# Kernel tuning notes

Measured on AMD Instinct MI355X. Metric: run time of the kernel, lower is better.

## Reference

```python
import jax, jax.numpy as jnp
import numpy as np

# Sizes
NC, NT, NP = 100000, 300000, 50000   # customers, transactions, products
F, DIMC = 8, 16                      # columns per table, per-column embed dim
D = F * DIMC                         # 128 = proj_dim (lazy SAGEConv in-channels)
L, R = 2, 4                          # gnn layers, relation types
OUT = 10                             # out_channels
EM, EI = 300000, 600000              # edges: customer-makes-transaction, product-in-transaction


def setup_inputs() -> dict:
    key = jax.random.key(0)
    ks = jax.random.split(key, 14)
    s = 0.05
    return {
        "x_c": jax.random.normal(ks[0], (NC, F), jnp.float32),
        "x_t": jax.random.normal(ks[1], (NT, F), jnp.float32),
        "x_p": jax.random.normal(ks[2], (NP, F), jnp.float32),
        # per-table per-column numeric embedders: scalar -> DIMC (w*x + b)
        "W_col": jax.random.normal(ks[3], (3, F, DIMC), jnp.float32) * s,
        "b_col": jax.random.normal(ks[4], (3, F, DIMC), jnp.float32) * s,
        # SAGEConv weights per layer per relation: lin_l (neighbor) and lin_r (root)
        "Wn": jax.random.normal(ks[5], (L, R, D, D), jnp.float32) * s,
        "Wr": jax.random.normal(ks[6], (L, R, D, D), jnp.float32) * s,
        "b_lin": jax.random.normal(ks[7], (L, R, D), jnp.float32) * s,
        "W_out": jax.random.normal(ks[8], (D, OUT), jnp.float32) * s,
        "b_out": jax.random.normal(ks[9], (OUT,), jnp.float32) * s,
        "e_makes_src": jax.random.randint(ks[10], (EM,), 0, NC, jnp.int32),
        "e_makes_dst": jax.random.randint(ks[11], (EM,), 0, NT, jnp.int32),
        "e_in_src": jax.random.randint(ks[12], (EI,), 0, NP, jnp.int32),
        "e_in_dst": jax.random.randint(ks[13], (EI,), 0, NT, jnp.int32),
    }


def _embed(x, W, b):
    # x: [N, F]; W,b: [F, DIMC] -> [N, F*DIMC] (concat of per-column embeddings)
    n = x.shape[0]
    return (x[:, :, None] * W[None] + b[None]).reshape(n, -1)


def _sage(x_src, x_dst, src, dst, Wn, Wr, b, n_dst):
    # SAGEConv(mean): out = mean_neigh(x_src) @ Wn + b + x_dst @ Wr
    msg = jax.ops.segment_sum(x_src[src], dst, num_segments=n_dst)
    cnt = jax.ops.segment_sum(jnp.ones(src.shape[0], x_src.dtype), dst, num_segments=n_dst)
    mean = msg / jnp.maximum(cnt, 1.0)[:, None]  # isolated nodes -> 0 message
    return mean @ Wn + x_dst @ Wr + b


def reference(x_c, x_t, x_p, W_col, b_col, Wn, Wr, b_lin, W_out, b_out,
              e_makes_src, e_makes_dst, e_in_src, e_in_dst):
    h_c = _embed(x_c, W_col[0], b_col[0])
    h_t = _embed(x_t, W_col[1], b_col[1])
    h_p = _embed(x_p, W_col[2], b_col[2])
    for l in range(L):
        # R0: customer -makes-> transaction
        o_t0 = _sage(h_c, h_t, e_makes_src, e_makes_dst, Wn[l, 0], Wr[l, 0], b_lin[l, 0], NT)
        # R1: transaction -rev_makes-> customer
        o_c = _sage(h_t, h_c, e_makes_dst, e_makes_src, Wn[l, 1], Wr[l, 1], b_lin[l, 1], NC)
        # R2: product -in-> transaction
        o_t2 = _sage(h_p, h_t, e_in_src, e_in_dst, Wn[l, 2], Wr[l, 2], b_lin[l, 2], NT)
        # R3: transaction -rev_in-> product
        o_p = _sage(h_t, h_p, e_in_dst, e_in_src, Wn[l, 3], Wr[l, 3], b_lin[l, 3], NP)
        # HeteroConv(aggr='mean'): mean over relations targeting each dst type
        h_c, h_t, h_p = o_c, 0.5 * (o_t0 + o_t2), o_p
    logits = h_t @ W_out + b_out  # target_table = 'transaction'
    return jax.nn.softmax(logits, axis=1)
```

## Files before the change

kernel.cpp:

```cpp
#include <hip/hip_runtime.h>

#define NCV 100000
#define NTV 300000
#define NPV 50000
#define DD 128
#define OUTC 10
#define EMV 300000
#define EIV 600000
#define YST 16

__global__ __launch_bounds__(256) void prep_T_w(
    const float* __restrict__ Wn10, const float* __restrict__ Wn12,
    const float* __restrict__ Wr10, const float* __restrict__ Wr12,
    const float* __restrict__ Wout, float* __restrict__ T) {
  int gw = (blockIdx.x * 256 + threadIdx.x) >> 6;
  int lane = threadIdx.x & 63;
  if (gw >= 3 * 1280) return;
  int mat = gw / 1280, r = gw % 1280, n = r / 10, o = r % 10;
  float s = 0.f;
  #pragma unroll
  for (int mi = 0; mi < 2; ++mi) {
    int m = lane + mi * 64;
    float w;
    if (mat == 0) w = Wn10[n * 128 + m];
    else if (mat == 1) w = Wn12[n * 128 + m];
    else w = 0.5f * (Wr10[n * 128 + m] + Wr12[n * 128 + m]);
    s += w * Wout[m * 10 + o];
  }
  #pragma unroll
  for (int d = 32; d; d >>= 1) s += __shfl_xor(s, d);
  if (lane == 0) T[gw] = s;
}

__global__ __launch_bounds__(256) void prep_Q_w(
    const float* __restrict__ Wn01, const float* __restrict__ Wr01,
    const float* __restrict__ Wn03, const float* __restrict__ Wr03,
    const float* __restrict__ Wn00, const float* __restrict__ Wn02,
    const float* __restrict__ Wr00, const float* __restrict__ Wr02,
    const float* __restrict__ T, float* __restrict__ Q) {
  int gw = (blockIdx.x * 256 + threadIdx.x) >> 6;
  int lane = threadIdx.x & 63;
  if (gw >= 7 * 1280) return;
  int q = gw / 1280, r = gw % 1280, k = r / 10, o = r % 10;
  const float* T1 = T, *T2 = T + 1280, *T3 = T + 2560;
  float s = 0.f;
  #pragma unroll
  for (int ni = 0; ni < 2; ++ni) {
    int n = lane + ni * 64;
    float w, t;
    switch (q) {
      case 0: w = Wn01[k * 128 + n]; t = T1[n * 10 + o]; break;
      case 1: w = Wr01[k * 128 + n]; t = T1[n * 10 + o]; break;
      case 2: w = Wn03[k * 128 + n]; t = T2[n * 10 + o]; break;
      case 3: w = Wr03[k * 128 + n]; t = T2[n * 10 + o]; break;
      case 4: w = Wn00[k * 128 + n]; t = T3[n * 10 + o]; break;
      case 5: w = Wn02[k * 128 + n]; t = T3[n * 10 + o]; break;
      default: w = Wr00[k * 128 + n] + Wr02[k * 128 + n]; t = T3[n * 10 + o]; break;
    }
    s += w * t;
  }
  #pragma unroll
  for (int d = 32; d; d >>= 1) s += __shfl_xor(s, d);
  if (lane == 0) Q[gw] = s;
}

__global__ __launch_bounds__(256) void prep_B_w(
    const float* __restrict__ Wcol, const float* __restrict__ bcol,
    const float* __restrict__ b_lin, const float* __restrict__ Wout,
    const float* __restrict__ bout, const float* __restrict__ T,
    const float* __restrict__ Q, float* __restrict__ B) {
  int gw = (blockIdx.x * 256 + threadIdx.x) >> 6;
  int lane = threadIdx.x & 63;
  if (gw >= 450) return;
  int r = gw / 10, o = gw % 10;
  const float* WcC = Wcol, *WcT = Wcol + 128, *WcP = Wcol + 256;
  const float* bC = bcol, *bT = bcol + 128, *bP = bcol + 256;
  const float* Q1 = Q, *Q2 = Q + 1280, *Q3 = Q + 2560, *Q4 = Q + 3840;
  const float* Q5 = Q + 5120, *Q6 = Q + 6400, *Q7 = Q + 7680;
  const float* T1 = T, *T2 = T + 1280, *T3 = T + 2560;
  const float* b00 = b_lin, *b01 = b_lin + 128, *b02 = b_lin + 256, *b03 = b_lin + 384;
  const float* b10 = b_lin + 512, *b12 = b_lin + 768;
  float s = 0.f;
  if (r < 8) {
    if (lane < 16) s = WcT[r * 16 + lane] * Q1[(r * 16 + lane) * 10 + o];
  } else if (r < 16) {
    int j = r - 8;
    if (lane < 16)
      s = WcC[j * 16 + lane] * (Q2[(j * 16 + lane) * 10 + o] + Q5[(j * 16 + lane) * 10 + o]);
  } else if (r == 16) {
    for (int k2 = lane; k2 < 128; k2 += 64) s += bT[k2] * Q1[k2 * 10 + o];
  } else if (r < 25) {
    int j = r - 17;
    if (lane < 16) s = WcT[j * 16 + lane] * Q3[(j * 16 + lane) * 10 + o];
  } else if (r < 33) {
    int j = r - 25;
    if (lane < 16)
      s = WcP[j * 16 + lane] * (Q4[(j * 16 + lane) * 10 + o] + Q6[(j * 16 + lane) * 10 + o]);
  } else if (r == 33) {
    for (int k2 = lane; k2 < 128; k2 += 64) s += bT[k2] * Q3[k2 * 10 + o];
  } else if (r < 42) {
    int j = r - 34;
    if (lane < 16) s = WcT[j * 16 + lane] * Q7[(j * 16 + lane) * 10 + o];
  } else if (r == 42) {
    for (int k2 = lane; k2 < 128; k2 += 64)
      s += bC[k2] * (Q2[k2 * 10 + o] + Q5[k2 * 10 + o]) + b01[k2] * T1[k2 * 10 + o];
  } else if (r == 43) {
    for (int k2 = lane; k2 < 128; k2 += 64)
      s += bP[k2] * (Q4[k2 * 10 + o] + Q6[k2 * 10 + o]) + b03[k2] * T2[k2 * 10 + o];
  } else {
    for (int n = lane; n < 128; n += 64)
      s += (b10[n] + b12[n]) * Wout[n * 10 + o] + bT[n] * Q7[n * 10 + o] +
           (b00[n] + b02[n]) * T3[n * 10 + o];
  }
  #pragma unroll
  for (int d = 32; d; d >>= 1) s += __shfl_xor(s, d);
  if (lane == 0) {
    float v = s * 0.5f;
    if (r == 44) v += bout[o];
    B[gw] = v;
  }
}

__global__ __launch_bounds__(256) void build_lists(
    const int* __restrict__ ems, const int* __restrict__ emd,
    const int* __restrict__ eis, const int* __restrict__ eid,
    int* __restrict__ head_c, int* __restrict__ head_tm,
    int* __restrict__ head_p, int* __restrict__ head_ti,
    int* __restrict__ nxt_mc, int* __restrict__ nxt_mt,
    int* __restrict__ nxt_ip, int* __restrict__ nxt_it) {
  int e = blockIdx.x * 256 + threadIdx.x;
  if (e < EMV) {
    int c = ems[e], t = emd[e];
    nxt_mc[e] = atomicExch(&head_c[c], e);
    nxt_mt[e] = atomicExch(&head_tm[t], e);
  }
  if (e < EIV) {
    int p = eis[e], t = eid[e];
    nxt_ip[e] = atomicExch(&head_p[p], e);
    nxt_it[e] = atomicExch(&head_ti[t], e);
  }
}

__global__ __launch_bounds__(256) void gather_y(
    const float* __restrict__ xt,
    const int* __restrict__ emd, const int* __restrict__ eid,
    const int* __restrict__ head_c, const int* __restrict__ head_p,
    const int* __restrict__ nxt_mc, const int* __restrict__ nxt_ip,
    const float* __restrict__ xc, const float* __restrict__ xp,
    const float* __restrict__ B,
    float* __restrict__ y_c, float* __restrict__ y_p) {
  __shared__ float sB[340];
  int tid = threadIdx.x;
  for (int i = tid; i < 340; i += 256) sB[i] = B[i];
  __syncthreads();
  int i = blockIdx.x * 256 + tid;
  if (i >= NCV + NPV) return;
  bool isC = i < NCV;
  int idx = isC ? i : i - NCV;
  const int* dstA = isC ? emd : eid;
  const int* nxt = isC ? nxt_mc : nxt_ip;
  int e = isC ? head_c[idx] : head_p[idx];

  float acc[8] = {0.f, 0.f, 0.f, 0.f, 0.f, 0.f, 0.f, 0.f};
  float cnt = 0.f;
  while (e >= 0) {
    const float4* xr = (const float4*)(xt + (size_t)dstA[e] * 8);
    float4 u = xr[0], v = xr[1];
    acc[0] += u.x; acc[1] += u.y; acc[2] += u.z; acc[3] += u.w;
    acc[4] += v.x; acc[5] += v.y; acc[6] += v.z; acc[7] += v.w;
    cnt += 1.f;
    e = nxt[e];
  }

  const float* xo = (isC ? xc : xp) + (size_t)idx * 8;
  const float* Bs = sB + (isC ? 0 : 170);
  float g = cnt > 0.f ? 1.f : 0.f;
  float inv = g / fmaxf(cnt, 1.f);
  float lg[OUTC];
  #pragma unroll
  for (int o = 0; o < OUTC; ++o) lg[o] = g * Bs[16 * 10 + o];
  #pragma unroll
  for (int r = 0; r < 8; ++r) {
    float zb = acc[r] * inv;
    float zo = xo[r];
    #pragma unroll
    for (int o = 0; o < OUTC; ++o)
      lg[o] += zb * Bs[r * 10 + o] + zo * Bs[(8 + r) * 10 + o];
  }
  float* y = (isC ? y_c : y_p) + (size_t)idx * YST;
  #pragma unroll
  for (int o = 0; o < OUTC; ++o) y[o] = lg[o];
}

__global__ __launch_bounds__(256) void gather_t(
    const float* __restrict__ y_c, const float* __restrict__ y_p,
    const float* __restrict__ xt,
    const int* __restrict__ ems, const int* __restrict__ eis,
    const int* __restrict__ head_tm, const int* __restrict__ head_ti,
    const int* __restrict__ nxt_mt, const int* __restrict__ nxt_it,
    const float* __restrict__ B, float* __restrict__ out) {
  __shared__ float sB[110];
  int tid = threadIdx.x;
  for (int i = tid; i < 110; i += 256) sB[i] = B[340 + i];
  __syncthreads();
  int t = blockIdx.x * 256 + tid;
  if (t >= NTV) return;

  float sc[OUTC] = {0.f, 0.f, 0.f, 0.f, 0.f, 0.f, 0.f, 0.f, 0.f, 0.f};
  float sp[OUTC] = {0.f, 0.f, 0.f, 0.f, 0.f, 0.f, 0.f, 0.f, 0.f, 0.f};
  float dc = 0.f, dp = 0.f;
  for (int e = head_tm[t]; e >= 0; e = nxt_mt[e]) {
    const float* yr = y_c + (size_t)ems[e] * YST;
    float4 u = *(const float4*)yr;
    float4 v = *(const float4*)(yr + 4);
    float2 w = *(const float2*)(yr + 8);
    sc[0] += u.x; sc[1] += u.y; sc[2] += u.z; sc[3] += u.w;
    sc[4] += v.x; sc[5] += v.y; sc[6] += v.z; sc[7] += v.w;
    sc[8] += w.x; sc[9] += w.y;
    dc += 1.f;
  }
  for (int e = head_ti[t]; e >= 0; e = nxt_it[e]) {
    const float* yr = y_p + (size_t)eis[e] * YST;
    float4 u = *(const float4*)yr;
    float4 v = *(const float4*)(yr + 4);
    float2 w = *(const float2*)(yr + 8);
    sp[0] += u.x; sp[1] += u.y; sp[2] += u.z; sp[3] += u.w;
    sp[4] += v.x; sp[5] += v.y; sp[6] += v.z; sp[7] += v.w;
    sp[8] += w.x; sp[9] += w.y;
    dp += 1.f;
  }

  float Gc = dc > 0.f ? 1.f : 0.f, Gp = dp > 0.f ? 1.f : 0.f;
  float ivc = 1.f / fmaxf(dc, 1.f), ivp = 1.f / fmaxf(dp, 1.f);

  const float4* xp4 = (const float4*)(xt + (size_t)t * 8);
  float4 xa = xp4[0], xb = xp4[1];
  float xv[8] = {xa.x, xa.y, xa.z, xa.w, xb.x, xb.y, xb.z, xb.w};

  float lg[OUTC];
  #pragma unroll
  for (int o = 0; o < OUTC; ++o)
    lg[o] = sc[o] * ivc + sp[o] * ivp +
            Gc * sB[80 + o] + Gp * sB[90 + o] + sB[100 + o];
  #pragma unroll
  for (int r = 0; r < 8; ++r) {
    float xr = xv[r];
    #pragma unroll
    for (int o = 0; o < OUTC; ++o) lg[o] += xr * sB[r * 10 + o];
  }

  float m = lg[0];
  #pragma unroll
  for (int o = 1; o < OUTC; ++o) m = fmaxf(m, lg[o]);
  float s = 0.f;
  #pragma unroll
  for (int o = 0; o < OUTC; ++o) { lg[o] = __expf(lg[o] - m); s += lg[o]; }
  float invs = 1.0f / s;
  float* op = &out[(size_t)t * OUTC];
  #pragma unroll
  for (int o = 0; o < 5; ++o) {
    float2 p2; p2.x = lg[2 * o] * invs; p2.y = lg[2 * o + 1] * invs;
    *(float2*)&op[2 * o] = p2;
  }
}

extern "C" void kernel_launch(void* const* d_in, const int* in_sizes, int n_in,
                              void* d_out, int out_size, void* d_ws, size_t ws_size,
                              hipStream_t stream) {
  const float* x_c   = (const float*)d_in[0];
  const float* x_t   = (const float*)d_in[1];
  const float* x_p   = (const float*)d_in[2];
  const float* W_col = (const float*)d_in[3];
  const float* b_col = (const float*)d_in[4];
  const float* Wn    = (const float*)d_in[5];
  const float* Wr    = (const float*)d_in[6];
  const float* b_lin = (const float*)d_in[7];
  const float* W_out = (const float*)d_in[8];
  const float* b_out = (const float*)d_in[9];
  const int* e_m_src = (const int*)d_in[10];
  const int* e_m_dst = (const int*)d_in[11];
  const int* e_i_src = (const int*)d_in[12];
  const int* e_i_dst = (const int*)d_in[13];
  float* out = (float*)d_out;

  size_t cursor = 0;
  char* base = (char*)d_ws;
  auto alloc = [&](size_t bytes) {
    void* p = base + cursor;
    cursor += (bytes + 255) & ~(size_t)255;
    return p;
  };
  float* y_c  = (float*)alloc((size_t)NCV * YST * 4);
  float* y_p  = (float*)alloc((size_t)NPV * YST * 4);
  int* heads  = (int*)alloc((size_t)(NCV + NPV + 2 * NTV) * 4);
  int* head_c  = heads;
  int* head_p  = heads + NCV;
  int* head_tm = heads + NCV + NPV;
  int* head_ti = heads + NCV + NPV + NTV;
  int* nxt_mc = (int*)alloc((size_t)EMV * 4);
  int* nxt_mt = (int*)alloc((size_t)EMV * 4);
  int* nxt_ip = (int*)alloc((size_t)EIV * 4);
  int* nxt_it = (int*)alloc((size_t)EIV * 4);
  float* T    = (float*)alloc(3 * 1280 * 4);
  float* Q    = (float*)alloc(7 * 1280 * 4);
  float* B    = (float*)alloc(450 * 4);

  const float* Wn_l[2][4]; const float* Wr_l[2][4];
  for (int l = 0; l < 2; ++l)
    for (int r = 0; r < 4; ++r) {
      Wn_l[l][r] = Wn + (size_t)(l * 4 + r) * DD * DD;
      Wr_l[l][r] = Wr + (size_t)(l * 4 + r) * DD * DD;
    }

  hipMemsetAsync(heads, 0xFF, (size_t)(NCV + NPV + 2 * NTV) * 4, stream);

  prep_T_w<<<(3 * 1280 * 64 + 255) / 256, 256, 0, stream>>>(
      Wn_l[1][0], Wn_l[1][2], Wr_l[1][0], Wr_l[1][2], W_out, T);
  prep_Q_w<<<(7 * 1280 * 64 + 255) / 256, 256, 0, stream>>>(
      Wn_l[0][1], Wr_l[0][1], Wn_l[0][3], Wr_l[0][3],
      Wn_l[0][0], Wn_l[0][2], Wr_l[0][0], Wr_l[0][2], T, Q);
  prep_B_w<<<(450 * 64 + 255) / 256, 256, 0, stream>>>(
      W_col, b_col, b_lin, W_out, b_out, T, Q, B);

  build_lists<<<(EIV + 255) / 256, 256, 0, stream>>>(
      e_m_src, e_m_dst, e_i_src, e_i_dst,
      head_c, head_tm, head_p, head_ti,
      nxt_mc, nxt_mt, nxt_ip, nxt_it);

  gather_y<<<(NCV + NPV + 255) / 256, 256, 0, stream>>>(
      x_t, e_m_dst, e_i_dst, head_c, head_p, nxt_mc, nxt_ip,
      x_c, x_p, B, y_c, y_p);

  gather_t<<<(NTV + 255) / 256, 256, 0, stream>>>(
      y_c, y_p, x_t, e_m_src, e_i_src, head_tm, head_ti,
      nxt_mt, nxt_it, B, out);
}
```

Baseline: 245.0 us.

## Fuse weight folding and head init into one kernel; vectorize list building

```diff
diff --git a/kernel.cpp b/kernel.cpp
--- a/kernel.cpp
+++ b/kernel.cpp
@@ -3,121 +3,139 @@
 #define NCV 100000
 #define NTV 300000
 #define NPV 50000
-#define DD 128
 #define OUTC 10
 #define EMV 300000
 #define EIV 600000
 #define YST 16
 
-__global__ __launch_bounds__(256) void prep_T_w(
-    const float* __restrict__ Wn10, const float* __restrict__ Wn12,
-    const float* __restrict__ Wr10, const float* __restrict__ Wr12,
-    const float* __restrict__ Wout, float* __restrict__ T) {
-  int gw = (blockIdx.x * 256 + threadIdx.x) >> 6;
-  int lane = threadIdx.x & 63;
-  if (gw >= 3 * 1280) return;
-  int mat = gw / 1280, r = gw % 1280, n = r / 10, o = r % 10;
-  float s = 0.f;
-  #pragma unroll
-  for (int mi = 0; mi < 2; ++mi) {
-    int m = lane + mi * 64;
-    float w;
-    if (mat == 0) w = Wn10[n * 128 + m];
-    else if (mat == 1) w = Wn12[n * 128 + m];
-    else w = 0.5f * (Wr10[n * 128 + m] + Wr12[n * 128 + m]);
-    s += w * Wout[m * 10 + o];
-  }
-  #pragma unroll
-  for (int d = 32; d; d >>= 1) s += __shfl_xor(s, d);
-  if (lane == 0) T[gw] = s;
-}
-
-__global__ __launch_bounds__(256) void prep_Q_w(
-    const float* __restrict__ Wn01, const float* __restrict__ Wr01,
-    const float* __restrict__ Wn03, const float* __restrict__ Wr03,
-    const float* __restrict__ Wn00, const float* __restrict__ Wn02,
-    const float* __restrict__ Wr00, const float* __restrict__ Wr02,
-    const float* __restrict__ T, float* __restrict__ Q) {
-  int gw = (blockIdx.x * 256 + threadIdx.x) >> 6;
-  int lane = threadIdx.x & 63;
-  if (gw >= 7 * 1280) return;
-  int q = gw / 1280, r = gw % 1280, k = r / 10, o = r % 10;
-  const float* T1 = T, *T2 = T + 1280, *T3 = T + 2560;
-  float s = 0.f;
-  #pragma unroll
-  for (int ni = 0; ni < 2; ++ni) {
-    int n = lane + ni * 64;
-    float w, t;
-    switch (q) {
-      case 0: w = Wn01[k * 128 + n]; t = T1[n * 10 + o]; break;
-      case 1: w = Wr01[k * 128 + n]; t = T1[n * 10 + o]; break;
-      case 2: w = Wn03[k * 128 + n]; t = T2[n * 10 + o]; break;
-      case 3: w = Wr03[k * 128 + n]; t = T2[n * 10 + o]; break;
-      case 4: w = Wn00[k * 128 + n]; t = T3[n * 10 + o]; break;
-      case 5: w = Wn02[k * 128 + n]; t = T3[n * 10 + o]; break;
-      default: w = Wr00[k * 128 + n] + Wr02[k * 128 + n]; t = T3[n * 10 + o]; break;
+__global__ __launch_bounds__(256) void fold_init(
+    const float* __restrict__ Wcol, const float* __restrict__ bcol,
+    const float* __restrict__ Wn, const float* __restrict__ Wr,
+    const float* __restrict__ b_lin, const float* __restrict__ Wout,
+    const float* __restrict__ bout,
+    int* __restrict__ heads, int nheads, float* __restrict__ B) {
+  __shared__ float sWout[1280];
+  __shared__ float sT[3840];
+  __shared__ float sQ[8960];
+  int tid = threadIdx.x;
+
+  if (blockIdx.x != 0) {
+    int i = (blockIdx.x - 1) * 256 + tid;
+    int stride = (gridDim.x - 1) * 256;
+    for (; i < nheads; i += stride) heads[i] = -1;
+    return;
+  }
+
+  for (int i = tid; i < 1280; i += 256) sWout[i] = Wout[i];
+  __syncthreads();
+
+  const float* Wn00 = Wn;             const float* Wn01 = Wn + 1 * 16384;
+  const float* Wn02 = Wn + 2 * 16384; const float* Wn03 = Wn + 3 * 16384;
+  const float* Wn10 = Wn + 4 * 16384; const float* Wn12 = Wn + 6 * 16384;
+  const float* Wr00 = Wr;             const float* Wr01 = Wr + 1 * 16384;
+  const float* Wr02 = Wr + 2 * 16384; const float* Wr03 = Wr + 3 * 16384;
+  const float* Wr10 = Wr + 4 * 16384; const float* Wr12 = Wr + 6 * 16384;
+
+  for (int task = tid; task < 3 * 128; task += 256) {
+    int mat = task >> 7, n = task & 127;
+    float acc[10];
+    #pragma unroll
+    for (int o = 0; o < 10; ++o) acc[o] = 0.f;
+    for (int m = 0; m < 128; m += 4) {
+      float4 w4;
+      if (mat == 0) w4 = *(const float4*)(Wn10 + n * 128 + m);
+      else if (mat == 1) w4 = *(const float4*)(Wn12 + n * 128 + m);
+      else {
+        float4 a = *(const float4*)(Wr10 + n * 128 + m);
+        float4 b = *(const float4*)(Wr12 + n * 128 + m);
+        w4 = make_float4(0.5f * (a.x + b.x), 0.5f * (a.y + b.y),
+                         0.5f * (a.z + b.z), 0.5f * (a.w + b.w));
+      }
+      const float* wo = &sWout[m * 10];
+      #pragma unroll
+      for (int o = 0; o < 10; ++o)
+        acc[o] += w4.x * wo[o] + w4.y * wo[10 + o] + w4.z * wo[20 + o] + w4.w * wo[30 + o];
     }
-    s += w * t;
-  }
-  #pragma unroll
-  for (int d = 32; d; d >>= 1) s += __shfl_xor(s, d);
-  if (lane == 0) Q[gw] = s;
-}
-
-__global__ __launch_bounds__(256) void prep_B_w(
-    const float* __restrict__ Wcol, const float* __restrict__ bcol,
-    const float* __restrict__ b_lin, const float* __restrict__ Wout,
-    const float* __restrict__ bout, const float* __restrict__ T,
-    const float* __restrict__ Q, float* __restrict__ B) {
-  int gw = (blockIdx.x * 256 + threadIdx.x) >> 6;
-  int lane = threadIdx.x & 63;
-  if (gw >= 450) return;
-  int r = gw / 10, o = gw % 10;
+    #pragma unroll
+    for (int o = 0; o < 10; ++o) sT[task * 10 + o] = acc[o];
+  }
+  __syncthreads();
+
+  for (int task = tid; task < 7 * 128; task += 256) {
+    int q = task / 128, k = task & 127;
+    const float* Tsel = &sT[(q < 2 ? 0 : (q < 4 ? 1 : 2)) * 1280];
+    float acc[10];
+    #pragma unroll
+    for (int o = 0; o < 10; ++o) acc[o] = 0.f;
+    for (int n = 0; n < 128; n += 4) {
+      float4 w4;
+      switch (q) {
+        case 0: w4 = *(const float4*)(Wn01 + k * 128 + n); break;
+        case 1: w4 = *(const float4*)(Wr01 + k * 128 + n); break;
+        case 2: w4 = *(const float4*)(Wn03 + k * 128 + n); break;
+        case 3: w4 = *(const float4*)(Wr03 + k * 128 + n); break;
+        case 4: w4 = *(const float4*)(Wn00 + k * 128 + n); break;
+        case 5: w4 = *(const float4*)(Wn02 + k * 128 + n); break;
+        default: {
+          float4 a = *(const float4*)(Wr00 + k * 128 + n);
+          float4 b = *(const float4*)(Wr02 + k * 128 + n);
+          w4 = make_float4(a.x + b.x, a.y + b.y, a.z + b.z, a.w + b.w);
+        } break;
+      }
+      const float* tr = &Tsel[n * 10];
+      #pragma unroll
+      for (int o = 0; o < 10; ++o)
+        acc[o] += w4.x * tr[o] + w4.y * tr[10 + o] + w4.z * tr[20 + o] + w4.w * tr[30 + o];
+    }
+    #pragma unroll
+    for (int o = 0; o < 10; ++o) sQ[task * 10 + o] = acc[o];
+  }
+  __syncthreads();
+
   const float* WcC = Wcol, *WcT = Wcol + 128, *WcP = Wcol + 256;
   const float* bC = bcol, *bT = bcol + 128, *bP = bcol + 256;
-  const float* Q1 = Q, *Q2 = Q + 1280, *Q3 = Q + 2560, *Q4 = Q + 3840;
-  const float* Q5 = Q + 5120, *Q6 = Q + 6400, *Q7 = Q + 7680;
-  const float* T1 = T, *T2 = T + 1280, *T3 = T + 2560;
+  const float* Q1 = sQ, *Q2 = sQ + 1280, *Q3 = sQ + 2560, *Q4 = sQ + 3840;
+  const float* Q5 = sQ + 5120, *Q6 = sQ + 6400, *Q7 = sQ + 7680;
+  const float* T1 = sT, *T2 = sT + 1280, *T3 = sT + 2560;
   const float* b00 = b_lin, *b01 = b_lin + 128, *b02 = b_lin + 256, *b03 = b_lin + 384;
   const float* b10 = b_lin + 512, *b12 = b_lin + 768;
-  float s = 0.f;
-  if (r < 8) {
-    if (lane < 16) s = WcT[r * 16 + lane] * Q1[(r * 16 + lane) * 10 + o];
-  } else if (r < 16) {
-    int j = r - 8;
-    if (lane < 16)
-      s = WcC[j * 16 + lane] * (Q2[(j * 16 + lane) * 10 + o] + Q5[(j * 16 + lane) * 10 + o]);
-  } else if (r == 16) {
-    for (int k2 = lane; k2 < 128; k2 += 64) s += bT[k2] * Q1[k2 * 10 + o];
-  } else if (r < 25) {
-    int j = r - 17;
-    if (lane < 16) s = WcT[j * 16 + lane] * Q3[(j * 16 + lane) * 10 + o];
-  } else if (r < 33) {
-    int j = r - 25;
-    if (lane < 16)
-      s = WcP[j * 16 + lane] * (Q4[(j * 16 + lane) * 10 + o] + Q6[(j * 16 + lane) * 10 + o]);
-  } else if (r == 33) {
-    for (int k2 = lane; k2 < 128; k2 += 64) s += bT[k2] * Q3[k2 * 10 + o];
-  } else if (r < 42) {
-    int j = r - 34;
-    if (lane < 16) s = WcT[j * 16 + lane] * Q7[(j * 16 + lane) * 10 + o];
-  } else if (r == 42) {
-    for (int k2 = lane; k2 < 128; k2 += 64)
-      s += bC[k2] * (Q2[k2 * 10 + o] + Q5[k2 * 10 + o]) + b01[k2] * T1[k2 * 10 + o];
-  } else if (r == 43) {
-    for (int k2 = lane; k2 < 128; k2 += 64)
-      s += bP[k2] * (Q4[k2 * 10 + o] + Q6[k2 * 10 + o]) + b03[k2] * T2[k2 * 10 + o];
-  } else {
-    for (int n = lane; n < 128; n += 64)
-      s += (b10[n] + b12[n]) * Wout[n * 10 + o] + bT[n] * Q7[n * 10 + o] +
-           (b00[n] + b02[n]) * T3[n * 10 + o];
-  }
-  #pragma unroll
-  for (int d = 32; d; d >>= 1) s += __shfl_xor(s, d);
-  if (lane == 0) {
+  for (int task = tid; task < 450; task += 256) {
+    int r = task / 10, o = task % 10;
+    float s = 0.f;
+    if (r < 8) {
+      for (int j = 0; j < 16; ++j) s += WcT[r * 16 + j] * Q1[(r * 16 + j) * 10 + o];
+    } else if (r < 16) {
+      int jr = r - 8;
+      for (int j = 0; j < 16; ++j)
+        s += WcC[jr * 16 + j] * (Q2[(jr * 16 + j) * 10 + o] + Q5[(jr * 16 + j) * 10 + o]);
+    } else if (r == 16) {
+      for (int k2 = 0; k2 < 128; ++k2) s += bT[k2] * Q1[k2 * 10 + o];
+    } else if (r < 25) {
+      int jr = r - 17;
+      for (int j = 0; j < 16; ++j) s += WcT[jr * 16 + j] * Q3[(jr * 16 + j) * 10 + o];
+    } else if (r < 33) {
+      int jr = r - 25;
+      for (int j = 0; j < 16; ++j)
+        s += WcP[jr * 16 + j] * (Q4[(jr * 16 + j) * 10 + o] + Q6[(jr * 16 + j) * 10 + o]);
+    } else if (r == 33) {
+      for (int k2 = 0; k2 < 128; ++k2) s += bT[k2] * Q3[k2 * 10 + o];
+    } else if (r < 42) {
+      int jr = r - 34;
+      for (int j = 0; j < 16; ++j) s += WcT[jr * 16 + j] * Q7[(jr * 16 + j) * 10 + o];
+    } else if (r == 42) {
+      for (int k2 = 0; k2 < 128; ++k2)
+        s += bC[k2] * (Q2[k2 * 10 + o] + Q5[k2 * 10 + o]) + b01[k2] * T1[k2 * 10 + o];
+    } else if (r == 43) {
+      for (int k2 = 0; k2 < 128; ++k2)
+        s += bP[k2] * (Q4[k2 * 10 + o] + Q6[k2 * 10 + o]) + b03[k2] * T2[k2 * 10 + o];
+    } else {
+      for (int n = 0; n < 128; ++n)
+        s += (b10[n] + b12[n]) * sWout[n * 10 + o] + bT[n] * Q7[n * 10 + o] +
+             (b00[n] + b02[n]) * T3[n * 10 + o];
+    }
     float v = s * 0.5f;
     if (r == 44) v += bout[o];
-    B[gw] = v;
+    B[task] = v;
   }
 }
 
@@ -128,16 +146,37 @@
     int* __restrict__ head_p, int* __restrict__ head_ti,
     int* __restrict__ nxt_mc, int* __restrict__ nxt_mt,
     int* __restrict__ nxt_ip, int* __restrict__ nxt_it) {
-  int e = blockIdx.x * 256 + threadIdx.x;
-  if (e < EMV) {
-    int c = ems[e], t = emd[e];
-    nxt_mc[e] = atomicExch(&head_c[c], e);
-    nxt_mt[e] = atomicExch(&head_tm[t], e);
-  }
-  if (e < EIV) {
-    int p = eis[e], t = eid[e];
-    nxt_ip[e] = atomicExch(&head_p[p], e);
-    nxt_it[e] = atomicExch(&head_ti[t], e);
+  int g = blockIdx.x * 256 + threadIdx.x;
+  int e0 = g * 4;
+  if (e0 < EMV) {
+    int4 s = ((const int4*)ems)[g];
+    int4 d = ((const int4*)emd)[g];
+    int4 n0, n1;
+    n0.x = atomicExch(&head_c[s.x], e0);
+    n0.y = atomicExch(&head_c[s.y], e0 + 1);
+    n0.z = atomicExch(&head_c[s.z], e0 + 2);
+    n0.w = atomicExch(&head_c[s.w], e0 + 3);
+    n1.x = atomicExch(&head_tm[d.x], e0);
+    n1.y = atomicExch(&head_tm[d.y], e0 + 1);
+    n1.z = atomicExch(&head_tm[d.z], e0 + 2);
+    n1.w = atomicExch(&head_tm[d.w], e0 + 3);
+    ((int4*)nxt_mc)[g] = n0;
+    ((int4*)nxt_mt)[g] = n1;
+  }
+  if (e0 < EIV) {
+    int4 s = ((const int4*)eis)[g];
+    int4 d = ((const int4*)eid)[g];
+    int4 n0, n1;
+    n0.x = atomicExch(&head_p[s.x], e0);
+    n0.y = atomicExch(&head_p[s.y], e0 + 1);
+    n0.z = atomicExch(&head_p[s.z], e0 + 2);
+    n0.w = atomicExch(&head_p[s.w], e0 + 3);
+    n1.x = atomicExch(&head_ti[d.x], e0);
+    n1.y = atomicExch(&head_ti[d.y], e0 + 1);
+    n1.z = atomicExch(&head_ti[d.z], e0 + 2);
+    n1.w = atomicExch(&head_ti[d.w], e0 + 3);
+    ((int4*)nxt_ip)[g] = n0;
+    ((int4*)nxt_it)[g] = n1;
   }
 }
 
@@ -292,7 +331,8 @@
   };
   float* y_c  = (float*)alloc((size_t)NCV * YST * 4);
   float* y_p  = (float*)alloc((size_t)NPV * YST * 4);
-  int* heads  = (int*)alloc((size_t)(NCV + NPV + 2 * NTV) * 4);
+  int nheads = NCV + NPV + 2 * NTV;
+  int* heads  = (int*)alloc((size_t)nheads * 4);
   int* head_c  = heads;
   int* head_p  = heads + NCV;
   int* head_tm = heads + NCV + NPV;
@@ -301,28 +341,12 @@
   int* nxt_mt = (int*)alloc((size_t)EMV * 4);
   int* nxt_ip = (int*)alloc((size_t)EIV * 4);
   int* nxt_it = (int*)alloc((size_t)EIV * 4);
-  float* T    = (float*)alloc(3 * 1280 * 4);
-  float* Q    = (float*)alloc(7 * 1280 * 4);
   float* B    = (float*)alloc(450 * 4);
 
-  const float* Wn_l[2][4]; const float* Wr_l[2][4];
-  for (int l = 0; l < 2; ++l)
-    for (int r = 0; r < 4; ++r) {
-      Wn_l[l][r] = Wn + (size_t)(l * 4 + r) * DD * DD;
-      Wr_l[l][r] = Wr + (size_t)(l * 4 + r) * DD * DD;
-    }
-
-  hipMemsetAsync(heads, 0xFF, (size_t)(NCV + NPV + 2 * NTV) * 4, stream);
-
-  prep_T_w<<<(3 * 1280 * 64 + 255) / 256, 256, 0, stream>>>(
-      Wn_l[1][0], Wn_l[1][2], Wr_l[1][0], Wr_l[1][2], W_out, T);
-  prep_Q_w<<<(7 * 1280 * 64 + 255) / 256, 256, 0, stream>>>(
-      Wn_l[0][1], Wr_l[0][1], Wn_l[0][3], Wr_l[0][3],
-      Wn_l[0][0], Wn_l[0][2], Wr_l[0][0], Wr_l[0][2], T, Q);
-  prep_B_w<<<(450 * 64 + 255) / 256, 256, 0, stream>>>(
-      W_col, b_col, b_lin, W_out, b_out, T, Q, B);
-
-  build_lists<<<(EIV + 255) / 256, 256, 0, stream>>>(
+  fold_init<<<129, 256, 0, stream>>>(
+      W_col, b_col, Wn, Wr, b_lin, W_out, b_out, heads, nheads, B);
+
+  build_lists<<<(EIV / 4 + 255) / 256, 256, 0, stream>>>(
       e_m_src, e_m_dst, e_i_src, e_i_dst,
       head_c, head_tm, head_p, head_ti,
       nxt_mc, nxt_mt, nxt_ip, nxt_it);
```

New measurement: 315.9 us. +28.9%, slower.

## Pack next-pointer and neighbor id into int2 linked-list nodes, interleave transaction traversals

Applied to the files above, without the earlier changes.

```diff
diff --git a/kernel.cpp b/kernel.cpp
--- a/kernel.cpp
+++ b/kernel.cpp
@@ -121,31 +121,34 @@
   }
 }
 
-__global__ __launch_bounds__(256) void build_lists(
+__global__ __launch_bounds__(256) void build_graph(
     const int* __restrict__ ems, const int* __restrict__ emd,
     const int* __restrict__ eis, const int* __restrict__ eid,
-    int* __restrict__ head_c, int* __restrict__ head_tm,
-    int* __restrict__ head_p, int* __restrict__ head_ti,
-    int* __restrict__ nxt_mc, int* __restrict__ nxt_mt,
-    int* __restrict__ nxt_ip, int* __restrict__ nxt_it) {
+    int* __restrict__ head_c, int* __restrict__ head_p,
+    int* __restrict__ heads_t,
+    int2* __restrict__ cn_m, int2* __restrict__ tn_m,
+    int2* __restrict__ pn_i, int2* __restrict__ tn_i) {
   int e = blockIdx.x * 256 + threadIdx.x;
   if (e < EMV) {
     int c = ems[e], t = emd[e];
-    nxt_mc[e] = atomicExch(&head_c[c], e);
-    nxt_mt[e] = atomicExch(&head_tm[t], e);
+    int cn = atomicExch(&head_c[c], e);
+    int tn = atomicExch(&heads_t[2 * t], e);
+    cn_m[e] = make_int2(cn, t);
+    tn_m[e] = make_int2(tn, c);
   }
   if (e < EIV) {
     int p = eis[e], t = eid[e];
-    nxt_ip[e] = atomicExch(&head_p[p], e);
-    nxt_it[e] = atomicExch(&head_ti[t], e);
+    int pn = atomicExch(&head_p[p], e);
+    int tn = atomicExch(&heads_t[2 * t + 1], e);
+    pn_i[e] = make_int2(pn, t);
+    tn_i[e] = make_int2(tn, p);
   }
 }
 
 __global__ __launch_bounds__(256) void gather_y(
     const float* __restrict__ xt,
-    const int* __restrict__ emd, const int* __restrict__ eid,
     const int* __restrict__ head_c, const int* __restrict__ head_p,
-    const int* __restrict__ nxt_mc, const int* __restrict__ nxt_ip,
+    const int2* __restrict__ cn_m, const int2* __restrict__ pn_i,
     const float* __restrict__ xc, const float* __restrict__ xp,
     const float* __restrict__ B,
     float* __restrict__ y_c, float* __restrict__ y_p) {
@@ -157,28 +160,28 @@
   if (i >= NCV + NPV) return;
   bool isC = i < NCV;
   int idx = isC ? i : i - NCV;
-  const int* dstA = isC ? emd : eid;
-  const int* nxt = isC ? nxt_mc : nxt_ip;
+  const int2* nodes = isC ? cn_m : pn_i;
   int e = isC ? head_c[idx] : head_p[idx];
 
   float acc[8] = {0.f, 0.f, 0.f, 0.f, 0.f, 0.f, 0.f, 0.f};
   float cnt = 0.f;
   while (e >= 0) {
-    const float4* xr = (const float4*)(xt + (size_t)dstA[e] * 8);
-    float4 u = xr[0], v = xr[1];
+    int2 v = nodes[e];
+    const float4* xr = (const float4*)(xt + (size_t)v.y * 8);
+    float4 u = xr[0], w = xr[1];
     acc[0] += u.x; acc[1] += u.y; acc[2] += u.z; acc[3] += u.w;
-    acc[4] += v.x; acc[5] += v.y; acc[6] += v.z; acc[7] += v.w;
+    acc[4] += w.x; acc[5] += w.y; acc[6] += w.z; acc[7] += w.w;
     cnt += 1.f;
-    e = nxt[e];
+    e = v.x;
   }
 
   const float* xo = (isC ? xc : xp) + (size_t)idx * 8;
   const float* Bs = sB + (isC ? 0 : 170);
-  float g = cnt > 0.f ? 1.f : 0.f;
-  float inv = g / fmaxf(cnt, 1.f);
+  float gg = cnt > 0.f ? 1.f : 0.f;
+  float inv = gg / fmaxf(cnt, 1.f);
   float lg[OUTC];
   #pragma unroll
-  for (int o = 0; o < OUTC; ++o) lg[o] = g * Bs[16 * 10 + o];
+  for (int o = 0; o < OUTC; ++o) lg[o] = gg * Bs[16 * 10 + o];
   #pragma unroll
   for (int r = 0; r < 8; ++r) {
     float zb = acc[r] * inv;
@@ -187,17 +190,18 @@
     for (int o = 0; o < OUTC; ++o)
       lg[o] += zb * Bs[r * 10 + o] + zo * Bs[(8 + r) * 10 + o];
   }
-  float* y = (isC ? y_c : y_p) + (size_t)idx * YST;
-  #pragma unroll
-  for (int o = 0; o < OUTC; ++o) y[o] = lg[o];
+  float4* yv = (float4*)((isC ? y_c : y_p) + (size_t)idx * YST);
+  yv[0] = make_float4(lg[0], lg[1], lg[2], lg[3]);
+  yv[1] = make_float4(lg[4], lg[5], lg[6], lg[7]);
+  yv[2] = make_float4(lg[8], lg[9], 0.f, 0.f);
+  yv[3] = make_float4(0.f, 0.f, 0.f, 0.f);
 }
 
 __global__ __launch_bounds__(256) void gather_t(
     const float* __restrict__ y_c, const float* __restrict__ y_p,
     const float* __restrict__ xt,
-    const int* __restrict__ ems, const int* __restrict__ eis,
-    const int* __restrict__ head_tm, const int* __restrict__ head_ti,
-    const int* __restrict__ nxt_mt, const int* __restrict__ nxt_it,
+    const int* __restrict__ heads_t,
+    const int2* __restrict__ tn_m, const int2* __restrict__ tn_i,
     const float* __restrict__ B, float* __restrict__ out) {
   __shared__ float sB[110];
   int tid = threadIdx.x;
@@ -206,28 +210,37 @@
   int t = blockIdx.x * 256 + tid;
   if (t >= NTV) return;
 
+  int2 ht = ((const int2*)heads_t)[t];
+  int e1 = ht.x, e2 = ht.y;
+
   float sc[OUTC] = {0.f, 0.f, 0.f, 0.f, 0.f, 0.f, 0.f, 0.f, 0.f, 0.f};
   float sp[OUTC] = {0.f, 0.f, 0.f, 0.f, 0.f, 0.f, 0.f, 0.f, 0.f, 0.f};
   float dc = 0.f, dp = 0.f;
-  for (int e = head_tm[t]; e >= 0; e = nxt_mt[e]) {
-    const float* yr = y_c + (size_t)ems[e] * YST;
-    float4 u = *(const float4*)yr;
-    float4 v = *(const float4*)(yr + 4);
-    float2 w = *(const float2*)(yr + 8);
-    sc[0] += u.x; sc[1] += u.y; sc[2] += u.z; sc[3] += u.w;
-    sc[4] += v.x; sc[5] += v.y; sc[6] += v.z; sc[7] += v.w;
-    sc[8] += w.x; sc[9] += w.y;
-    dc += 1.f;
-  }
-  for (int e = head_ti[t]; e >= 0; e = nxt_it[e]) {
-    const float* yr = y_p + (size_t)eis[e] * YST;
-    float4 u = *(const float4*)yr;
-    float4 v = *(const float4*)(yr + 4);
-    float2 w = *(const float2*)(yr + 8);
-    sp[0] += u.x; sp[1] += u.y; sp[2] += u.z; sp[3] += u.w;
-    sp[4] += v.x; sp[5] += v.y; sp[6] += v.z; sp[7] += v.w;
-    sp[8] += w.x; sp[9] += w.y;
-    dp += 1.f;
+  while (e1 >= 0 || e2 >= 0) {
+    if (e1 >= 0) {
+      int2 v = tn_m[e1];
+      const float* yr = y_c + (size_t)v.y * YST;
+      float4 u = *(const float4*)yr;
+      float4 w = *(const float4*)(yr + 4);
+      float2 z = *(const float2*)(yr + 8);
+      sc[0] += u.x; sc[1] += u.y; sc[2] += u.z; sc[3] += u.w;
+      sc[4] += w.x; sc[5] += w.y; sc[6] += w.z; sc[7] += w.w;
+      sc[8] += z.x; sc[9] += z.y;
+      dc += 1.f;
+      e1 = v.x;
+    }
+    if (e2 >= 0) {
+      int2 v = tn_i[e2];
+      const float* yr = y_p + (size_t)v.y * YST;
+      float4 u = *(const float4*)yr;
+      float4 w = *(const float4*)(yr + 4);
+      float2 z = *(const float2*)(yr + 8);
+      sp[0] += u.x; sp[1] += u.y; sp[2] += u.z; sp[3] += u.w;
+      sp[4] += w.x; sp[5] += w.y; sp[6] += w.z; sp[7] += w.w;
+      sp[8] += z.x; sp[9] += z.y;
+      dp += 1.f;
+      e2 = v.x;
+    }
   }
 
   float Gc = dc > 0.f ? 1.f : 0.f, Gp = dp > 0.f ? 1.f : 0.f;
@@ -290,20 +303,20 @@
     cursor += (bytes + 255) & ~(size_t)255;
     return p;
   };
-  float* y_c  = (float*)alloc((size_t)NCV * YST * 4);
-  float* y_p  = (float*)alloc((size_t)NPV * YST * 4);
-  int* heads  = (int*)alloc((size_t)(NCV + NPV + 2 * NTV) * 4);
+  int nheads = NCV + NPV + 2 * NTV;
+  int* heads   = (int*)alloc((size_t)nheads * 4);
   int* head_c  = heads;
   int* head_p  = heads + NCV;
-  int* head_tm = heads + NCV + NPV;
-  int* head_ti = heads + NCV + NPV + NTV;
-  int* nxt_mc = (int*)alloc((size_t)EMV * 4);
-  int* nxt_mt = (int*)alloc((size_t)EMV * 4);
-  int* nxt_ip = (int*)alloc((size_t)EIV * 4);
-  int* nxt_it = (int*)alloc((size_t)EIV * 4);
-  float* T    = (float*)alloc(3 * 1280 * 4);
-  float* Q    = (float*)alloc(7 * 1280 * 4);
-  float* B    = (float*)alloc(450 * 4);
+  int* heads_t = heads + NCV + NPV;
+  int2* cn_m = (int2*)alloc((size_t)EMV * 8);
+  int2* tn_m = (int2*)alloc((size_t)EMV * 8);
+  int2* pn_i = (int2*)alloc((size_t)EIV * 8);
+  int2* tn_i = (int2*)alloc((size_t)EIV * 8);
+  float* y_c = (float*)alloc((size_t)NCV * YST * 4);
+  float* y_p = (float*)alloc((size_t)NPV * YST * 4);
+  float* T   = (float*)alloc(3 * 1280 * 4);
+  float* Q   = (float*)alloc(7 * 1280 * 4);
+  float* B   = (float*)alloc(450 * 4);
 
   const float* Wn_l[2][4]; const float* Wr_l[2][4];
   for (int l = 0; l < 2; ++l)
@@ -312,7 +325,11 @@
       Wr_l[l][r] = Wr + (size_t)(l * 4 + r) * DD * DD;
     }
 
-  hipMemsetAsync(heads, 0xFF, (size_t)(NCV + NPV + 2 * NTV) * 4, stream);
+  hipMemsetAsync(heads, 0xFF, (size_t)nheads * 4, stream);
+
+  build_graph<<<(EIV + 255) / 256, 256, 0, stream>>>(
+      e_m_src, e_m_dst, e_i_src, e_i_dst,
+      head_c, head_p, heads_t, cn_m, tn_m, pn_i, tn_i);
 
   prep_T_w<<<(3 * 1280 * 64 + 255) / 256, 256, 0, stream>>>(
       Wn_l[1][0], Wn_l[1][2], Wr_l[1][0], Wr_l[1][2], W_out, T);
@@ -322,16 +339,9 @@
   prep_B_w<<<(450 * 64 + 255) / 256, 256, 0, stream>>>(
       W_col, b_col, b_lin, W_out, b_out, T, Q, B);
 
-  build_lists<<<(EIV + 255) / 256, 256, 0, stream>>>(
-      e_m_src, e_m_dst, e_i_src, e_i_dst,
-      head_c, head_tm, head_p, head_ti,
-      nxt_mc, nxt_mt, nxt_ip, nxt_it);
-
   gather_y<<<(NCV + NPV + 255) / 256, 256, 0, stream>>>(
-      x_t, e_m_dst, e_i_dst, head_c, head_p, nxt_mc, nxt_ip,
-      x_c, x_p, B, y_c, y_p);
+      x_t, head_c, head_p, cn_m, pn_i, x_c, x_p, B, y_c, y_p);
 
   gather_t<<<(NTV + 255) / 256, 256, 0, stream>>>(
-      y_c, y_p, x_t, e_m_src, e_i_src, head_tm, head_ti,
-      nxt_mt, nxt_it, B, out);
-}
+      y_c, y_p, x_t, heads_t, tn_m, tn_i, B, out);
+}
```

Measured after the change: 236.5 us. -3.5%, faster.
